# Kernel optimization log

Hardware: AMD Instinct MI355X
Metric: run time of the kernel (lower is better)

The kernel has to match this reference:

```python
import jax, jax.numpy as jnp
import numpy as np

L = 2048
E = 1024
H = 16
D = E // H


def setup_inputs() -> dict:
    key = jax.random.key(0)
    ks = jax.random.split(key, 9)
    inp = {
        "values": jax.random.normal(ks[0], (L, E), dtype=jnp.float32),
        "keys": jax.random.normal(ks[1], (L, E), dtype=jnp.float32),
        "query": jax.random.normal(ks[2], (L, E), dtype=jnp.float32),
        "dist_matrix": jax.random.uniform(ks[3], (L, L), dtype=jnp.float32),
        "Wv": jax.random.normal(ks[4], (E, E), dtype=jnp.float32) * 0.02,
        "Wk": jax.random.normal(ks[5], (E, E), dtype=jnp.float32) * 0.02,
        "Wq": jax.random.normal(ks[6], (E, E), dtype=jnp.float32) * 0.02,
        "Wo": jax.random.normal(ks[7], (E, E), dtype=jnp.float32) * 0.02,
        "bo": jax.random.normal(ks[8], (E,), dtype=jnp.float32) * 0.02,
    }
    return inp


def reference(values, keys, query, dist_matrix, Wv, Wk, Wq, Wo, bo):
    # Linear projections (torch Linear: x @ W.T), then split heads: [L, H, D]
    v = (values @ Wv.T).reshape(L, H, D)
    k = (keys @ Wk.T).reshape(L, H, D)
    q = (query @ Wq.T).reshape(L, H, D)

    # energy: [H, Lq, Lk]
    energy = jnp.einsum("qhd,khd->hqk", q, k)

    # distance bias: zeros -> inf, then 1/(d+1); broadcast over heads
    dm = jnp.where(dist_matrix == 0, jnp.inf, dist_matrix)
    bias = 1.0 / (dm + 1.0)
    energy = energy + bias[None, :, :]

    attn = jax.nn.softmax(energy / jnp.sqrt(jnp.float32(E)), axis=2)

    out = jnp.einsum("hql,lhd->qhd", attn, v).reshape(L, H * D)
    return out @ Wo.T + bo
```

## Files before the change

### kernel.cpp

```cpp
#include <hip/hip_runtime.h>


#define L_SEQ 2048
#define E_DIM 1024
#define H_HEADS 16
#define D_HEAD 64
#define KSPLIT 4
#define OSPLIT 2

typedef unsigned short u16;
typedef unsigned int u32;
typedef __attribute__((ext_vector_type(8))) short bf16x8;
typedef __attribute__((ext_vector_type(4))) short bf16x4;
typedef __attribute__((ext_vector_type(8))) unsigned short u16x8;
typedef __attribute__((ext_vector_type(4))) unsigned short u16x4;
typedef __attribute__((ext_vector_type(4))) float f32x4;

#define C_LOG2E_32 0.045084220027780106f

__device__ __forceinline__ float bf2f(u16 u) {
  union { u32 i; float f; } v; v.i = ((u32)u) << 16; return v.f;
}
__device__ __forceinline__ u16 f2bf(float f) {
  union { float f; u32 i; } v; v.f = f;
  u32 u = v.i;
  u += 0x7FFFu + ((u >> 16) & 1u);
  return (u16)(u >> 16);
}
__device__ __forceinline__ u32 pack_bf16_pair(float lo, float hi) {
  union { float f; u32 u; } a, b;
  a.f = lo; b.f = hi;
  return __builtin_amdgcn_perm(b.u + 0x8000u, a.u + 0x8000u, 0x07060302u);
}
__device__ __forceinline__ void gload16(const u16* g, u16* l) {
  __builtin_amdgcn_global_load_lds(
      (const __attribute__((address_space(1))) u32*)g,
      (__attribute__((address_space(3))) u32*)l, 16, 0, 0);
}

__global__ void cvt_all(const float* __restrict__ xq, const float* __restrict__ xk,
                        const float* __restrict__ xv,
                        const float* __restrict__ wq, const float* __restrict__ wk,
                        const float* __restrict__ wv, const float* __restrict__ wo,
                        const float* __restrict__ dist, const float* __restrict__ bo,
                        u16* oq, u16* ok, u16* ov,
                        u16* owq, u16* owk, u16* owv, u16* owo, u16* obias,
                        float* __restrict__ outp)
{
  size_t gid = (size_t)blockIdx.x * 256 + threadIdx.x;
  const size_t NQ = 262144;
  const size_t NW = 131072;
  const size_t DL = 524288;
  const size_t FILL = 3 * NQ + 4 * NW + DL;

  if (gid >= FILL) {
    size_t off = (gid - FILL) * 8;
    int n = (int)(off & (E_DIM - 1));
    *(f32x4*)&outp[off] = *(const f32x4*)&bo[n];
    *(f32x4*)&outp[off + 4] = *(const f32x4*)&bo[n + 4];
    return;
  }

  const float* src; u16* dst; size_t off; bool isb = false;
  if      (gid <     NQ)           { src = xq;   dst = oq;    off = gid; }
  else if (gid < 2 * NQ)           { src = xk;   dst = ok;    off = gid - NQ; }
  else if (gid < 3 * NQ)           { src = xv;   dst = ov;    off = gid - 2 * NQ; }
  else if (gid < 3 * NQ + NW)      { src = wq;   dst = owq;   off = gid - 3 * NQ; }
  else if (gid < 3 * NQ + 2 * NW)  { src = wk;   dst = owk;   off = gid - 3 * NQ - NW; }
  else if (gid < 3 * NQ + 3 * NW)  { src = wv;   dst = owv;   off = gid - 3 * NQ - 2 * NW; }
  else if (gid < 3 * NQ + 4 * NW)  { src = wo;   dst = owo;   off = gid - 3 * NQ - 3 * NW; }
  else { src = dist; dst = obias; off = gid - 3 * NQ - 4 * NW; isb = true; }

  f32x4 v0 = *(const f32x4*)&src[off * 8];
  f32x4 v1 = *(const f32x4*)&src[off * 8 + 4];
  u16x8 o;
#pragma unroll
  for (int j = 0; j < 4; ++j) {
    float f0 = v0[j], f1 = v1[j];
    if (isb) {
      f0 = (f0 == 0.f) ? 0.f : C_LOG2E_32 / (f0 + 1.f);
      f1 = (f1 == 0.f) ? 0.f : C_LOG2E_32 / (f1 + 1.f);
    }
    o[j] = f2bf(f0); o[j + 4] = f2bf(f1);
  }
  *(u16x8*)&dst[off * 8] = o;
}

#define TM 128
#define TN 128
#define BK 32

template<int OUTMODE>
__global__ __launch_bounds__(256, 3) void gemm_pd(
    const u16* __restrict__ A0, const u16* __restrict__ B0, void* __restrict__ C0,
    const u16* __restrict__ A1, const u16* __restrict__ B1, void* __restrict__ C1,
    const u16* __restrict__ A2, const u16* __restrict__ B2, void* __restrict__ C2,
    int M, int N, int K)
{
  const u16* A; const u16* B; void* C;
  if (OUTMODE == 2)         { A = A0; B = B0; C = C0; }
  else if (blockIdx.z == 0) { A = A0; B = B0; C = C0; }
  else if (blockIdx.z == 1) { A = A1; B = B1; C = C1; }
  else                      { A = A2; B = B2; C = C2; }

  __shared__ __align__(16) u16 As[2][TM * BK];
  __shared__ __align__(16) u16 Bs[2][TN * BK];

  const int m0 = blockIdx.y * TM;
  const int n0 = blockIdx.x * TN;
  const int t = threadIdx.x;
  const int wave = t >> 6;
  const int lane = t & 63;
  const int quad = lane >> 4;
  const int col  = lane & 15;
  const int wm = (wave >> 1) * 64;
  const int wn = (wave & 1) * 64;

  const int sr = lane >> 2;
  const int sg = ((lane & 3) ^ ((lane >> 3) & 3)) * 8;
  const u16* gA = A + (size_t)(m0 + wave * 32 + sr) * K + sg;
  const u16* gB = B + (size_t)(n0 + wave * 32 + sr) * K + sg;
  const int lo0 = (wave * 32) * BK;
  const int lo1 = (wave * 32 + 16) * BK;

  const int kbeg = (OUTMODE == 2) ? blockIdx.z * (K / OSPLIT) : 0;
  const int kend = (OUTMODE == 2) ? kbeg + K / OSPLIT : K;

  f32x4 acc[4][4];
#pragma unroll
  for (int i = 0; i < 4; ++i)
#pragma unroll
    for (int j = 0; j < 4; ++j) acc[i][j] = (f32x4){0.f, 0.f, 0.f, 0.f};

  gload16(gA + kbeg, &As[0][lo0]);
  gload16(gA + (size_t)16 * K + kbeg, &As[0][lo1]);
  gload16(gB + kbeg, &Bs[0][lo0]);
  gload16(gB + (size_t)16 * K + kbeg, &Bs[0][lo1]);

  const int slot8 = (quad ^ ((col >> 1) & 3)) * 8;

  int buf = 0;
  for (int k0 = kbeg; k0 < kend; k0 += BK) {
    __syncthreads();
    int nk = k0 + BK;
    if (nk < kend) {
      gload16(gA + nk, &As[buf ^ 1][lo0]);
      gload16(gA + (size_t)16 * K + nk, &As[buf ^ 1][lo1]);
      gload16(gB + nk, &Bs[buf ^ 1][lo0]);
      gload16(gB + (size_t)16 * K + nk, &Bs[buf ^ 1][lo1]);
    }

    bf16x8 af[4], bfr[4];
#pragma unroll
    for (int i = 0; i < 4; ++i)
      af[i] = *(const bf16x8*)&As[buf][(wm + i * 16 + col) * BK + slot8];
#pragma unroll
    for (int j = 0; j < 4; ++j)
      bfr[j] = *(const bf16x8*)&Bs[buf][(wn + j * 16 + col) * BK + slot8];

#pragma unroll
    for (int i = 0; i < 4; ++i)
#pragma unroll
      for (int j = 0; j < 4; ++j)
        acc[i][j] = __builtin_amdgcn_mfma_f32_16x16x32_bf16(af[i], bfr[j], acc[i][j], 0, 0, 0);

    buf ^= 1;
  }

  const bool transC = (OUTMODE == 0) && (blockIdx.z == 2);
#pragma unroll
  for (int i = 0; i < 4; ++i) {
    int rowb = m0 + wm + i * 16 + quad * 4;
#pragma unroll
    for (int j = 0; j < 4; ++j) {
      int cn = n0 + wn + j * 16 + col;
      if (OUTMODE == 2) {
#pragma unroll
        for (int r = 0; r < 4; ++r)
          unsafeAtomicAdd(&((float*)C)[(size_t)(rowb + r) * N + cn], acc[i][j][r]);
      } else if (transC) {
        u16x4 pk;
#pragma unroll
        for (int r = 0; r < 4; ++r) pk[r] = f2bf(acc[i][j][r]);
        *(u16x4*)&((u16*)C)[(size_t)cn * M + rowb] = pk;
      } else {
#pragma unroll
        for (int r = 0; r < 4; ++r)
          ((u16*)C)[(size_t)(rowb + r) * N + cn] = f2bf(acc[i][j][r]);
      }
    }
  }
}

#define FK 32

__global__ __launch_bounds__(256, 4) void flash8(
    const u16* __restrict__ Q, const u16* __restrict__ Kp,
    const u16* __restrict__ Vt, const u16* __restrict__ Bb,
    u16* __restrict__ Op, float* __restrict__ lp)
{
  __shared__ __align__(16) u16 Ks[2][FK * 64];
  __shared__ __align__(16) u16 Vs[2][D_HEAD * FK];

  const int h  = blockIdx.y;
  const int q0 = blockIdx.x * 128;
  const int z  = blockIdx.z;
  const int hoff = h * D_HEAD;
  const int kbase = z * (L_SEQ / KSPLIT);
  const int NT = (L_SEQ / KSPLIT) / FK;
  const int t = threadIdx.x;
  const int wave = t >> 6;
  const int lane = t & 63;
  const int quad = lane >> 4;
  const int col  = lane & 15;

  bf16x8 qf[2][2];
  const u16* brow[2];
#pragma unroll
  for (int s = 0; s < 2; ++s) {
    const int qs = q0 + wave * 32 + s * 16;
    const u16* qrow = Q + (size_t)(qs + col) * E_DIM + hoff;
    qf[s][0] = *(const bf16x8*)(qrow + quad * 8);
    qf[s][1] = *(const bf16x8*)(qrow + 32 + quad * 8);
    brow[s] = Bb + (size_t)(qs + col) * L_SEQ;
  }

  const int krow = wave * 8 + (lane >> 3);
  const int kg = ((lane & 7) ^ (lane >> 3)) * 8;
  const u16* gK = Kp + (size_t)krow * E_DIM + hoff + kg;
  const int vrow = wave * 16 + (lane >> 2);
  const int vg = ((lane & 3) ^ ((lane >> 4) & 3)) * 8;
  const u16* gV = Vt + (size_t)(hoff + vrow) * L_SEQ + vg;

  float l_lane[2] = {0.f, 0.f};
  f32x4 oacc[2][4];
#pragma unroll
  for (int s = 0; s < 2; ++s)
#pragma unroll
    for (int td = 0; td < 4; ++td) oacc[s][td] = (f32x4){0.f, 0.f, 0.f, 0.f};

  gload16(gK + (size_t)kbase * E_DIM, &Ks[0][wave * 8 * 64]);
  gload16(gV + kbase, &Vs[0][wave * 16 * FK]);
  u16x4 bv[2][2], bn[2][2];
#pragma unroll
  for (int s = 0; s < 2; ++s) {
    bv[s][0] = *(const u16x4*)&brow[s][kbase + quad * 4];
    bv[s][1] = *(const u16x4*)&brow[s][kbase + 16 + quad * 4];
  }

  const int ks0 = (quad ^ (col & 7)) * 8;
  const int ks1 = ((quad + 4) ^ (col & 7)) * 8;
  const int vc2 = (col >> 2) & 3;
  const int vq1 = quad >> 1;
  const int vlo = (quad & 1) * 4;

  int buf = 0;
  for (int kt = 0; kt < NT; ++kt) {
    const int k0 = kbase + kt * FK;
    __syncthreads();
    if (kt + 1 < NT) {
      const int nk = k0 + FK;
      gload16(gK + (size_t)nk * E_DIM, &Ks[buf ^ 1][wave * 8 * 64]);
      gload16(gV + nk, &Vs[buf ^ 1][wave * 16 * FK]);
#pragma unroll
      for (int s = 0; s < 2; ++s) {
        bn[s][0] = *(const u16x4*)&brow[s][nk + quad * 4];
        bn[s][1] = *(const u16x4*)&brow[s][nk + 16 + quad * 4];
      }
    }
    const u16* Kb = &Ks[buf][0];
    const u16* Vb = &Vs[buf][0];

    bf16x4 vf[2][4];
#pragma unroll
    for (int tt = 0; tt < 2; ++tt) {
      const int slot = (tt * 2 + vq1) ^ vc2;
#pragma unroll
      for (int td = 0; td < 4; ++td)
        vf[tt][td] = *(const bf16x4*)&Vb[(td * 16 + col) * FK + slot * 8 + vlo];
    }

    bf16x4 pa[2][2];
#pragma unroll
    for (int tt = 0; tt < 2; ++tt) {
      const u16* kr = &Kb[(tt * 16 + col) * 64];
      bf16x8 kf0 = *(const bf16x8*)&kr[ks0];
      bf16x8 kf1 = *(const bf16x8*)&kr[ks1];
#pragma unroll
      for (int s = 0; s < 2; ++s) {
        f32x4 a = (f32x4){0.f, 0.f, 0.f, 0.f};
        a = __builtin_amdgcn_mfma_f32_16x16x32_bf16(kf0, qf[s][0], a, 0, 0, 0);
        a = __builtin_amdgcn_mfma_f32_16x16x32_bf16(kf1, qf[s][1], a, 0, 0, 0);
        float p[4];
#pragma unroll
        for (int r = 0; r < 4; ++r) {
          p[r] = __builtin_amdgcn_exp2f(fmaf(a[r], C_LOG2E_32, bf2f(bv[s][tt][r])));
          l_lane[s] += p[r];
        }
        union { u32 w[2]; bf16x4 v; } pk;
        pk.w[0] = pack_bf16_pair(p[0], p[1]);
        pk.w[1] = pack_bf16_pair(p[2], p[3]);
        pa[s][tt] = pk.v;
      }
    }

#pragma unroll
    for (int s = 0; s < 2; ++s)
#pragma unroll
      for (int td = 0; td < 4; ++td) {
        oacc[s][td] = __builtin_amdgcn_mfma_f32_16x16x16bf16_1k(
            pa[s][0], vf[0][td], oacc[s][td], 0, 0, 0);
        oacc[s][td] = __builtin_amdgcn_mfma_f32_16x16x16bf16_1k(
            pa[s][1], vf[1][td], oacc[s][td], 0, 0, 0);
      }

#pragma unroll
    for (int s = 0; s < 2; ++s) { bv[s][0] = bn[s][0]; bv[s][1] = bn[s][1]; }
    buf ^= 1;
  }

#pragma unroll
  for (int s = 0; s < 2; ++s) {
    l_lane[s] += __shfl_xor(l_lane[s], 16);
    l_lane[s] += __shfl_xor(l_lane[s], 32);
    if (lane < 16)
      lp[((size_t)z * L_SEQ + q0 + wave * 32 + s * 16 + lane) * H_HEADS + h] = l_lane[s];
  }

#pragma unroll
  for (int s = 0; s < 2; ++s) {
    const int qrow_mine = q0 + wave * 32 + s * 16 + quad * 4;
#pragma unroll
    for (int td = 0; td < 4; ++td)
#pragma unroll
      for (int r = 0; r < 4; ++r)
        Op[((size_t)z * L_SEQ + qrow_mine + r) * E_DIM + hoff + td * 16 + col] = f2bf(oacc[s][td][r]);
  }
}

__global__ void merge_attn(const u16* __restrict__ Op, const float* __restrict__ lp,
                           u16* __restrict__ AOb)
{
  size_t gid = (size_t)blockIdx.x * 256 + threadIdx.x;
  size_t idx = gid * 4;
  int q = (int)(idx >> 10);
  int e = (int)(idx & 1023);
  int h = e >> 6;
  float o[4] = {0.f, 0.f, 0.f, 0.f};
  float lsum = 0.f;
#pragma unroll
  for (int s = 0; s < KSPLIT; ++s) {
    u16x4 pv = *(const u16x4*)&Op[((size_t)s * L_SEQ + q) * E_DIM + e];
#pragma unroll
    for (int j = 0; j < 4; ++j) o[j] += bf2f(pv[j]);
    lsum += lp[((size_t)s * L_SEQ + q) * H_HEADS + h];
  }
  float inv = 1.f / lsum;
  u16x4 pk;
#pragma unroll
  for (int j = 0; j < 4; ++j) pk[j] = f2bf(o[j] * inv);
  *(u16x4*)&AOb[idx] = pk;
}

extern "C" void kernel_launch(void* const* d_in, const int* in_sizes, int n_in,
                              void* d_out, int out_size, void* d_ws, size_t ws_size,
                              hipStream_t stream)
{
  const float* values = (const float*)d_in[0];
  const float* keys   = (const float*)d_in[1];
  const float* query  = (const float*)d_in[2];
  const float* dist   = (const float*)d_in[3];
  const float* Wv     = (const float*)d_in[4];
  const float* Wk     = (const float*)d_in[5];
  const float* Wq     = (const float*)d_in[6];
  const float* Wo     = (const float*)d_in[7];
  const float* bo     = (const float*)d_in[8];
  float* out = (float*)d_out;

  const size_t MB = (size_t)1 << 20;
  char* w = (char*)d_ws;
  u16* xq  = (u16*)(w + 0 * MB);
  u16* xk  = (u16*)(w + 4 * MB);
  u16* xv  = (u16*)(w + 8 * MB);
  u16* wqb = (u16*)(w + 12 * MB);
  u16* wkb = (u16*)(w + 14 * MB);
  u16* wvb = (u16*)(w + 16 * MB);
  u16* wob = (u16*)(w + 18 * MB);
  u16* Bb  = (u16*)(w + 20 * MB);
  u16* Qh  = (u16*)(w + 28 * MB);
  u16* Kh  = (u16*)(w + 32 * MB);
  u16* Vth = (u16*)(w + 36 * MB);
  u16* AOb = (u16*)(w + 40 * MB);
  float* lp = (float*)(w + 44 * MB);
  u16* Op  = (u16*)(w + 0 * MB);

  cvt_all<<<8192, 256, 0, stream>>>(query, keys, values, Wq, Wk, Wv, Wo, dist, bo,
                                    xq, xk, xv, wqb, wkb, wvb, wob, Bb, out);

  dim3 gProj(E_DIM / TN, L_SEQ / TM, 3);
  gemm_pd<0><<<gProj, 256, 0, stream>>>(xq, wqb, Qh,
                                        xk, wkb, Kh,
                                        xv, wvb, Vth,
                                        L_SEQ, E_DIM, E_DIM);

  dim3 gAttn(L_SEQ / 128, H_HEADS, KSPLIT);
  flash8<<<gAttn, 256, 0, stream>>>(Qh, Kh, Vth, Bb, Op, lp);

  merge_attn<<<(L_SEQ * E_DIM / 4) / 256, 256, 0, stream>>>(Op, lp, AOb);

  dim3 gOut(E_DIM / TN, L_SEQ / TM, OSPLIT);
  gemm_pd<2><<<gOut, 256, 0, stream>>>(AOb, wob, out,
                                       AOb, wob, out,
                                       AOb, wob, out,
                                       L_SEQ, E_DIM, E_DIM);
}
```

Baseline: 210.1 us.

## Store distance bias in MFMA-fragment tiled layout and raise output GEMM split

The bf16 distance-bias matrix is now written in 16x16 tiles ordered so that each wave's 64 lanes read one contiguous 512-byte block. Before, each lane loaded 8 bytes from a different row, so the bias loads in the flash kernel were scattered. The conversion kernel gets a separate bias path with one thread per four elements, and its grid is enlarged to match. The output projection GEMM's split factor also changes from 2 to 4, which adds more blocks and more atomic-style partial accumulation into the output.

```diff
diff --git a/kernel.cpp b/kernel.cpp
--- a/kernel.cpp
+++ b/kernel.cpp
@@ -6,7 +6,7 @@
 #define H_HEADS 16
 #define D_HEAD 64
 #define KSPLIT 4
-#define OSPLIT 2
+#define OSPLIT 4
 
 typedef unsigned short u16;
 typedef unsigned int u32;
@@ -50,8 +50,27 @@
   size_t gid = (size_t)blockIdx.x * 256 + threadIdx.x;
   const size_t NQ = 262144;
   const size_t NW = 131072;
-  const size_t DL = 524288;
-  const size_t FILL = 3 * NQ + 4 * NW + DL;
+  const size_t DL2 = 1048576;
+  const size_t FILL = DL2 + 3 * NQ + 4 * NW;
+
+  if (gid < DL2) {
+    int tile = (int)(gid >> 6);
+    int ln   = (int)(gid & 63);
+    int l16  = tile >> 7;
+    int q16  = tile & 127;
+    int qq = q16 * 16 + (ln & 15);
+    int ll = l16 * 16 + (ln >> 4) * 4;
+    f32x4 d4 = *(const f32x4*)&dist[(size_t)qq * L_SEQ + ll];
+    u16x4 o4;
+#pragma unroll
+    for (int j = 0; j < 4; ++j) {
+      float f = d4[j];
+      f = (f == 0.f) ? 0.f : C_LOG2E_32 / (f + 1.f);
+      o4[j] = f2bf(f);
+    }
+    *(u16x4*)&obias[(size_t)tile * 256 + ln * 4] = o4;
+    return;
+  }
 
   if (gid >= FILL) {
     size_t off = (gid - FILL) * 8;
@@ -61,27 +80,22 @@
     return;
   }
 
-  const float* src; u16* dst; size_t off; bool isb = false;
-  if      (gid <     NQ)           { src = xq;   dst = oq;    off = gid; }
-  else if (gid < 2 * NQ)           { src = xk;   dst = ok;    off = gid - NQ; }
-  else if (gid < 3 * NQ)           { src = xv;   dst = ov;    off = gid - 2 * NQ; }
-  else if (gid < 3 * NQ + NW)      { src = wq;   dst = owq;   off = gid - 3 * NQ; }
-  else if (gid < 3 * NQ + 2 * NW)  { src = wk;   dst = owk;   off = gid - 3 * NQ - NW; }
-  else if (gid < 3 * NQ + 3 * NW)  { src = wv;   dst = owv;   off = gid - 3 * NQ - 2 * NW; }
-  else if (gid < 3 * NQ + 4 * NW)  { src = wo;   dst = owo;   off = gid - 3 * NQ - 3 * NW; }
-  else { src = dist; dst = obias; off = gid - 3 * NQ - 4 * NW; isb = true; }
+  size_t g = gid - DL2;
+  const float* src; u16* dst; size_t off;
+  if      (g <     NQ)           { src = xq;   dst = oq;    off = g; }
+  else if (g < 2 * NQ)           { src = xk;   dst = ok;    off = g - NQ; }
+  else if (g < 3 * NQ)           { src = xv;   dst = ov;    off = g - 2 * NQ; }
+  else if (g < 3 * NQ + NW)      { src = wq;   dst = owq;   off = g - 3 * NQ; }
+  else if (g < 3 * NQ + 2 * NW)  { src = wk;   dst = owk;   off = g - 3 * NQ - NW; }
+  else if (g < 3 * NQ + 3 * NW)  { src = wv;   dst = owv;   off = g - 3 * NQ - 2 * NW; }
+  else                           { src = wo;   dst = owo;   off = g - 3 * NQ - 3 * NW; }
 
   f32x4 v0 = *(const f32x4*)&src[off * 8];
   f32x4 v1 = *(const f32x4*)&src[off * 8 + 4];
   u16x8 o;
 #pragma unroll
   for (int j = 0; j < 4; ++j) {
-    float f0 = v0[j], f1 = v1[j];
-    if (isb) {
-      f0 = (f0 == 0.f) ? 0.f : C_LOG2E_32 / (f0 + 1.f);
-      f1 = (f1 == 0.f) ? 0.f : C_LOG2E_32 / (f1 + 1.f);
-    }
-    o[j] = f2bf(f0); o[j + 4] = f2bf(f1);
+    o[j] = f2bf(v0[j]); o[j + 4] = f2bf(v1[j]);
   }
   *(u16x8*)&dst[off * 8] = o;
 }
@@ -215,15 +229,15 @@
   const int col  = lane & 15;
 
   bf16x8 qf[2][2];
-  const u16* brow[2];
 #pragma unroll
   for (int s = 0; s < 2; ++s) {
     const int qs = q0 + wave * 32 + s * 16;
     const u16* qrow = Q + (size_t)(qs + col) * E_DIM + hoff;
     qf[s][0] = *(const bf16x8*)(qrow + quad * 8);
     qf[s][1] = *(const bf16x8*)(qrow + 32 + quad * 8);
-    brow[s] = Bb + (size_t)(qs + col) * L_SEQ;
-  }
+  }
+  const int qb0 = blockIdx.x * 8 + wave * 2;
+  const int lb4 = lane * 4;
 
   const int krow = wave * 8 + (lane >> 3);
   const int kg = ((lane & 7) ^ (lane >> 3)) * 8;
@@ -242,10 +256,13 @@
   gload16(gK + (size_t)kbase * E_DIM, &Ks[0][wave * 8 * 64]);
   gload16(gV + kbase, &Vs[0][wave * 16 * FK]);
   u16x4 bv[2][2], bn[2][2];
-#pragma unroll
-  for (int s = 0; s < 2; ++s) {
-    bv[s][0] = *(const u16x4*)&brow[s][kbase + quad * 4];
-    bv[s][1] = *(const u16x4*)&brow[s][kbase + 16 + quad * 4];
+  {
+    const int kb16 = kbase >> 4;
+#pragma unroll
+    for (int s = 0; s < 2; ++s) {
+      bv[s][0] = *(const u16x4*)&Bb[((size_t)(kb16 + 0) * 128 + qb0 + s) * 256 + lb4];
+      bv[s][1] = *(const u16x4*)&Bb[((size_t)(kb16 + 1) * 128 + qb0 + s) * 256 + lb4];
+    }
   }
 
   const int ks0 = (quad ^ (col & 7)) * 8;
@@ -262,10 +279,11 @@
       const int nk = k0 + FK;
       gload16(gK + (size_t)nk * E_DIM, &Ks[buf ^ 1][wave * 8 * 64]);
       gload16(gV + nk, &Vs[buf ^ 1][wave * 16 * FK]);
+      const int nk16 = nk >> 4;
 #pragma unroll
       for (int s = 0; s < 2; ++s) {
-        bn[s][0] = *(const u16x4*)&brow[s][nk + quad * 4];
-        bn[s][1] = *(const u16x4*)&brow[s][nk + 16 + quad * 4];
+        bn[s][0] = *(const u16x4*)&Bb[((size_t)(nk16 + 0) * 128 + qb0 + s) * 256 + lb4];
+        bn[s][1] = *(const u16x4*)&Bb[((size_t)(nk16 + 1) * 128 + qb0 + s) * 256 + lb4];
       }
     }
     const u16* Kb = &Ks[buf][0];
@@ -394,8 +412,8 @@
   float* lp = (float*)(w + 44 * MB);
   u16* Op  = (u16*)(w + 0 * MB);
 
-  cvt_all<<<8192, 256, 0, stream>>>(query, keys, values, Wq, Wk, Wv, Wo, dist, bo,
-                                    xq, xk, xv, wqb, wkb, wvb, wob, Bb, out);
+  cvt_all<<<10240, 256, 0, stream>>>(query, keys, values, Wq, Wk, Wv, Wo, dist, bo,
+                                     xq, xk, xv, wqb, wkb, wvb, wob, Bb, out);
 
   dim3 gProj(E_DIM / TN, L_SEQ / TM, 3);
   gemm_pd<0><<<gProj, 256, 0, stream>>>(xq, wqb, Qh,
```

Measured after the change: 206.5 us. About the same (-1.7%).
